# Optimization experiments

Measured on AMD Instinct MI355X. Metric: run time of the kernel, lower is better.

Reference implementation:

```python
import jax, jax.numpy as jnp
import numpy as np

N_HEADS = 8


def setup_inputs() -> dict:
    key = jax.random.key(0)
    k1, k2 = jax.random.split(key)
    image_qkv = jax.random.normal(k1, (2, 1536, 4096), dtype=jnp.float32)
    st_qkv = jax.random.normal(k2, (2, 1536, 1024), dtype=jnp.float32)
    return {"image_qkv": image_qkv, "st_qkv": st_qkv}


def reference(image_qkv, st_qkv):
    bs, width, img_len = image_qkv.shape
    st_len = st_qkv.shape[2]
    assert width % (3 * N_HEADS) == 0
    ch = width // (3 * N_HEADS)
    hc = N_HEADS * ch

    img_q, img_k, img_v = (image_qkv[:, i * hc:(i + 1) * hc] for i in range(3))
    st_q, st_k, st_v = (st_qkv[:, i * hc:(i + 1) * hc] for i in range(3))

    scale = 1.0 / jnp.sqrt(jnp.sqrt(jnp.float32(ch)))

    def split_heads(x, length):  # [bs, H*ch, L] -> [bs*H, ch, L]
        return x.reshape(bs * N_HEADS, ch, length)

    # image queries attend over st keys/values (softmax applied)
    w_i = jnp.einsum('bct,bcs->bts', split_heads(img_q, img_len) * scale,
                     split_heads(st_k, st_len) * scale)
    w_i = jax.nn.softmax(w_i.astype(jnp.float32), axis=-1).astype(w_i.dtype)
    attn_i = jnp.einsum('bts,bcs->bct', w_i, split_heads(st_v, st_len)).reshape(bs, -1, img_len)

    # st queries attend over image keys/values (NOTE: original code has NO softmax here)
    w_st = jnp.einsum('bct,bcs->bts', split_heads(st_q, st_len) * scale,
                      split_heads(img_k, img_len) * scale)
    attn_st = jnp.einsum('bts,bcs->bct', w_st, split_heads(img_v, img_len)).reshape(bs, -1, st_len)

    return attn_i, attn_st
```

## Files before the change

kernel.cpp:

```cpp
#include <hip/hip_runtime.h>
#include <hip/hip_bf16.h>
#include <stdint.h>

#define DEVI __device__ __forceinline__

typedef __attribute__((ext_vector_type(8))) short short8;
typedef __attribute__((ext_vector_type(16))) float f32x16;
typedef __attribute__((ext_vector_type(4))) float f32x4;
typedef __attribute__((ext_vector_type(2))) unsigned int uint2v;
typedef unsigned short ushortT;

union U8 { short8 s8; unsigned u[4]; };

DEVI unsigned short f2bf(float f) {
  unsigned u = __builtin_bit_cast(unsigned, f);
  u += 0x7fffu + ((u >> 16) & 1u);
  return (unsigned short)(u >> 16);
}
DEVI unsigned pk2(float lo, float hi) {
  return (unsigned)f2bf(lo) | ((unsigned)f2bf(hi) << 16);
}
DEVI unsigned cvtpk(float lo, float hi) {
  unsigned r;
  asm("v_cvt_pk_bf16_f32 %0, %1, %2" : "=v"(r) : "v"(lo), "v"(hi));
  return r;
}
DEVI float exp2a(float x) { return __builtin_amdgcn_exp2f(x); }

#define MFMA32 __builtin_amdgcn_mfma_f32_32x32x16_bf16
#define C_L2E 0.18033688011112042f

__global__ __launch_bounds__(256) void aux_kernel(
    const float* __restrict__ img, const float* __restrict__ st,
    ushortT* __restrict__ kfp, ushortT* __restrict__ vfp,
    float* __restrict__ Mws) {
  __shared__ __align__(16) char pool[32768];
  const int tid = threadIdx.x;
  const int bid = blockIdx.x;
  const int w = tid >> 6, lane = tid & 63, hi = lane >> 5, ln = lane & 31;

  if (bid < 256) {
    const int bh = bid >> 4, t = bid & 15;
    const int b = bh >> 3, h = bh & 7;
    const float* kbase = st + ((size_t)(b * 1536 + 512 + h * 64)) * 1024;
    const float* vbase = st + ((size_t)(b * 1536 + 1024 + h * 64)) * 1024;
    ushortT* ko = kfp + ((size_t)bh * 16 + t) * 4096;
    ushortT* vo = vfp + ((size_t)bh * 16 + t) * 4096;

    float (*kf)[65] = (float (*)[65])pool;
    {
      const int c = tid >> 2, s16 = (tid & 3) * 16;
      const float* kp = kbase + (size_t)c * 1024 + t * 64 + s16;
      f32x4 a = *(const f32x4*)kp, b4 = *(const f32x4*)(kp + 4),
            c4 = *(const f32x4*)(kp + 8), d4 = *(const f32x4*)(kp + 12);
#pragma unroll
      for (int j = 0; j < 4; ++j) {
        kf[c][s16 + j] = a[j];
        kf[c][s16 + 4 + j] = b4[j];
        kf[c][s16 + 8 + j] = c4[j];
        kf[c][s16 + 12 + j] = d4[j];
      }
    }
#pragma unroll
    for (int rep = 0; rep < 2; ++rep) {
      const int pair = tid + rep * 256;
      const int c = pair >> 3, oct = pair & 7;
      const float* vp = vbase + (size_t)c * 1024 + t * 64 + oct * 8;
      f32x4 lo = *(const f32x4*)vp, hp = *(const f32x4*)(vp + 4);
      uint2v la, ha;
      la[0] = pk2(lo[0], lo[1]); la[1] = pk2(lo[2], lo[3]);
      ha[0] = pk2(hp[0], hp[1]); ha[1] = pk2(hp[2], hp[3]);
      const int ci = c >> 5, lnn = c & 31;
      const int ss = oct >> 2, kk2 = (oct >> 1) & 1, o1 = oct & 1;
      const int f = ss * 4 + kk2 * 2 + ci;
      *(uint2v*)(vo + ((size_t)f * 64 + lnn) * 8 + o1 * 4) = la;
      *(uint2v*)(vo + ((size_t)f * 64 + 32 + lnn) * 8 + o1 * 4) = ha;
    }
    __syncthreads();
    {
      const int kk = w;
#pragma unroll
      for (int half = 0; half < 2; ++half) {
        float v8[8];
#pragma unroll
        for (int j = 0; j < 8; ++j) v8[j] = kf[kk * 16 + hi * 8 + j][half * 32 + ln];
        U8 u;
#pragma unroll
        for (int i = 0; i < 4; ++i) u.u[i] = pk2(v8[2 * i], v8[2 * i + 1]);
        *(short8*)(ko + ((size_t)(half * 4 + kk) * 64 + lane) * 8) = u.s8;
      }
    }
  } else {
    const int gb = bid - 256;
    const int bh = gb >> 3, chunk = gb & 7;
    const int b = bh >> 3, h = bh & 7;
    const float* kbase = img + ((size_t)(b * 1536 + 512 + h * 64)) * 4096;
    const float* vbase = img + ((size_t)(b * 1536 + 1024 + h * 64)) * 4096;

    f32x16 m00 = {}, m01 = {}, m10 = {}, m11 = {};
    const int sbeg = chunk * 512 + w * 128;
    for (int s0 = sbeg; s0 < sbeg + 128; s0 += 16) {
      const int sa = s0 + hi * 8;
      short8 av[2], bk[2];
#pragma unroll
      for (int ci = 0; ci < 2; ++ci) {
        const float* vp = vbase + (size_t)(ci * 32 + ln) * 4096 + sa;
        f32x4 lo = *(const f32x4*)vp, hp = *(const f32x4*)(vp + 4);
        U8 u;
        u.u[0] = pk2(lo[0], lo[1]); u.u[1] = pk2(lo[2], lo[3]);
        u.u[2] = pk2(hp[0], hp[1]); u.u[3] = pk2(hp[2], hp[3]);
        av[ci] = u.s8;
      }
#pragma unroll
      for (int cj = 0; cj < 2; ++cj) {
        const float* kp = kbase + (size_t)(cj * 32 + ln) * 4096 + sa;
        f32x4 lo = *(const f32x4*)kp, hp = *(const f32x4*)(kp + 4);
        U8 u;
        u.u[0] = pk2(lo[0], lo[1]); u.u[1] = pk2(lo[2], lo[3]);
        u.u[2] = pk2(hp[0], hp[1]); u.u[3] = pk2(hp[2], hp[3]);
        bk[cj] = u.s8;
      }
      m00 = MFMA32(av[0], bk[0], m00, 0, 0, 0);
      m01 = MFMA32(av[0], bk[1], m01, 0, 0, 0);
      m10 = MFMA32(av[1], bk[0], m10, 0, 0, 0);
      m11 = MFMA32(av[1], bk[1], m11, 0, 0, 0);
    }

    float (*part)[64][64] = (float (*)[64][64])pool;
    if (w < 2) {
#pragma unroll
      for (int q = 0; q < 16; ++q) {
        const int cr = (q & 3) + 8 * (q >> 2) + 4 * hi;
        part[w][cr][ln] = m00[q];
        part[w][cr][32 + ln] = m01[q];
        part[w][32 + cr][ln] = m10[q];
        part[w][32 + cr][32 + ln] = m11[q];
      }
    }
    __syncthreads();
    if (w >= 2) {
      const int pw = w - 2;
#pragma unroll
      for (int q = 0; q < 16; ++q) {
        const int cr = (q & 3) + 8 * (q >> 2) + 4 * hi;
        part[pw][cr][ln] += m00[q];
        part[pw][cr][32 + ln] += m01[q];
        part[pw][32 + cr][ln] += m10[q];
        part[pw][32 + cr][32 + ln] += m11[q];
      }
    }
    __syncthreads();
#pragma unroll
    for (int i = 0; i < 16; ++i) {
      const int e = tid + i * 256;
      const int c = e >> 6, cp = e & 63;
      Mws[(size_t)gb * 4096 + c * 64 + cp] =
          (part[0][c][cp] + part[1][c][cp]) * 0.125f;
    }
  }
}

DEVI void stage_tile(ushortT (*lds)[16][512], int buf, const ushortT* kf_all,
                     const ushortT* vf_all, int fpbase, int lane, int tile) {
#pragma unroll
  for (int j = 0; j < 4; ++j) {
    const int fp = fpbase + j;
    const ushortT* src =
        (fp < 8 ? kf_all + (size_t)tile * 4096 + (size_t)fp * 512
                : vf_all + (size_t)tile * 4096 + (size_t)(fp - 8) * 512) +
        lane * 8;
    __builtin_amdgcn_global_load_lds(
        (const __attribute__((address_space(1))) void*)src,
        (__attribute__((address_space(3))) void*)&lds[buf][fp][0], 16, 0, 0);
  }
}

DEVI void st2_body(const float* __restrict__ st, const float* __restrict__ Mws,
                   float* __restrict__ out1, int sb, int tid, char* pool) {
  const int bh = sb >> 2, tt = sb & 3;
  const int b = bh >> 3, h = bh & 7;
  const float* qbase = st + ((size_t)(b * 1536 + h * 64)) * 1024;
  float* o1 = out1 + ((size_t)(b * 512 + h * 64)) * 1024;
  char* msb = pool;

#pragma unroll
  for (int i = 0; i < 16; ++i) {
    const int e = tid + i * 256;
    const int c = e >> 6, cp = e & 63;
    const float* mp = Mws + (size_t)bh * 8 * 4096 + c * 64 + cp;
    float s = 0.f;
#pragma unroll
    for (int ch = 0; ch < 8; ++ch) s += mp[(size_t)ch * 4096];
    *(float*)(msb + c * 256 + ((cp * 4) ^ ((c & 7) << 5))) = s;
  }
  __syncthreads();

  const int w = tid >> 6, lane = tid & 63, hi = lane >> 5, ln = lane & 31;

  short8 aM0[4], aM1[4];
#pragma unroll
  for (int k = 0; k < 4; ++k) {
#pragma unroll
    for (int ci = 0; ci < 2; ++ci) {
      const int row = ci * 32 + ln;
      const int bo = k * 64 + hi * 32;
      const char* rp = msb + row * 256;
      const int swz = (row & 7) << 5;
      f32x4 lo = *(const f32x4*)(rp + (bo ^ swz));
      f32x4 hp = *(const f32x4*)(rp + ((bo + 16) ^ swz));
      U8 u;
      u.u[0] = pk2(lo[0], lo[1]); u.u[1] = pk2(lo[2], lo[3]);
      u.u[2] = pk2(hp[0], hp[1]); u.u[3] = pk2(hp[2], hp[3]);
      if (ci) aM1[k] = u.s8; else aM0[k] = u.s8;
    }
  }

#pragma unroll
  for (int nt = 0; nt < 2; ++nt) {
    const int t = tt * 256 + w * 64 + nt * 32 + ln;
    short8 bq[4];
#pragma unroll
    for (int k = 0; k < 4; ++k) {
      const float* qp = qbase + (size_t)(k * 16 + hi * 8) * 1024 + t;
      float q8[8];
#pragma unroll
      for (int j = 0; j < 8; ++j) q8[j] = qp[(size_t)j * 1024];
      U8 u;
#pragma unroll
      for (int i = 0; i < 4; ++i) u.u[i] = pk2(q8[2 * i], q8[2 * i + 1]);
      bq[k] = u.s8;
    }
    f32x16 a0 = {}, a1 = {};
#pragma unroll
    for (int k = 0; k < 4; ++k) {
      a0 = MFMA32(aM0[k], bq[k], a0, 0, 0, 0);
      a1 = MFMA32(aM1[k], bq[k], a1, 0, 0, 0);
    }
#pragma unroll
    for (int q = 0; q < 16; ++q) {
      const int cr = (q & 3) + 8 * (q >> 2) + 4 * hi;
      o1[(size_t)cr * 1024 + t] = a0[q];
      o1[(size_t)(cr + 32) * 1024 + t] = a1[q];
    }
  }
}

template <bool WITH_ST2>
__global__ __launch_bounds__(256, 2) void main_kernel(
    const float* __restrict__ img, const ushortT* __restrict__ kfp,
    const ushortT* __restrict__ vfp, const float* __restrict__ st,
    const float* __restrict__ Mws, float* __restrict__ out0,
    float* __restrict__ out1) {
  __shared__ __align__(16) char pool[65536];
  const int tid = threadIdx.x;
  const int bid = blockIdx.x;

  if (WITH_ST2 && bid >= 512) {
    st2_body(st, Mws, out1, bid - 512, tid, pool);
    return;
  }

  const int w = tid >> 6, lane = tid & 63, hi = lane >> 5, ln = lane & 31;
  const int bh = bid >> 5, tb = bid & 31;
  const int b = bh >> 3, h = bh & 7;
  const float* qbase = img + ((size_t)(b * 1536 + h * 64)) * 4096;
  float* obase = out0 + ((size_t)(b * 512 + h * 64)) * 4096;

  const int fpbase = w * 4;
  const int tcol = tb * 128 + w * 32 + ln;

  ushortT (*lds)[16][512] = (ushortT (*)[16][512])pool;
  const ushortT* kf_all = kfp + (size_t)bh * 16 * 4096;
  const ushortT* vf_all = vfp + (size_t)bh * 16 * 4096;

  stage_tile(lds, 0, kf_all, vf_all, fpbase, lane, 0);
  stage_tile(lds, 1, kf_all, vf_all, fpbase, lane, 1);
  stage_tile(lds, 2, kf_all, vf_all, fpbase, lane, 2);

  short8 qf[4];
#pragma unroll
  for (int k = 0; k < 4; ++k) {
    const float* qp = qbase + (size_t)(k * 16 + hi * 8) * 4096 + tcol;
    float q8[8];
#pragma unroll
    for (int j = 0; j < 8; ++j) q8[j] = qp[(size_t)j * 4096] * C_L2E;
    U8 u;
#pragma unroll
    for (int i = 0; i < 4; ++i) u.u[i] = pk2(q8[2 * i], q8[2 * i + 1]);
    qf[k] = u.s8;
  }

  f32x16 o0 = {}, o1 = {};
  float la0 = 0.f, la1 = 0.f, la2 = 0.f, la3 = 0.f;

  __syncthreads();

  for (int i = 0; i < 16; ++i) {
    if (i + 3 < 16)
      stage_tile(lds, (i + 3) & 3, kf_all, vf_all, fpbase, lane, i + 3);

    const ushortT(*L)[512] = lds[i & 3];

    f32x16 sc0 = {}, sc1 = {};
    {
      short8 kfr[8];
#pragma unroll
      for (int f = 0; f < 8; ++f) kfr[f] = *(const short8*)&L[f][lane * 8];
      __builtin_amdgcn_s_setprio(1);
      sc0 = MFMA32(kfr[0], qf[0], sc0, 0, 0, 0);
      sc1 = MFMA32(kfr[4], qf[0], sc1, 0, 0, 0);
      sc0 = MFMA32(kfr[1], qf[1], sc0, 0, 0, 0);
      sc1 = MFMA32(kfr[5], qf[1], sc1, 0, 0, 0);
      sc0 = MFMA32(kfr[2], qf[2], sc0, 0, 0, 0);
      sc1 = MFMA32(kfr[6], qf[2], sc1, 0, 0, 0);
      sc0 = MFMA32(kfr[3], qf[3], sc0, 0, 0, 0);
      sc1 = MFMA32(kfr[7], qf[3], sc1, 0, 0, 0);
      __builtin_amdgcn_s_setprio(0);
    }

#pragma unroll
    for (int q = 0; q < 16; q += 4) {
      float p0 = exp2a(sc0[q]);
      float p1 = exp2a(sc0[q + 1]);
      float p2 = exp2a(sc0[q + 2]);
      float p3 = exp2a(sc0[q + 3]);
      sc0[q] = p0; sc0[q + 1] = p1; sc0[q + 2] = p2; sc0[q + 3] = p3;
      la0 += p0; la1 += p1; la2 += p2; la3 += p3;
    }
#pragma unroll
    for (int q = 0; q < 16; q += 4) {
      float p0 = exp2a(sc1[q]);
      float p1 = exp2a(sc1[q + 1]);
      float p2 = exp2a(sc1[q + 2]);
      float p3 = exp2a(sc1[q + 3]);
      sc1[q] = p0; sc1[q + 1] = p1; sc1[q + 2] = p2; sc1[q + 3] = p3;
      la0 += p0; la1 += p1; la2 += p2; la3 += p3;
    }

#pragma unroll
    for (int ss = 0; ss < 2; ++ss) {
      const f32x16& sc = ss ? sc1 : sc0;
      U8 B0, B1;
      B0.u[0] = cvtpk(sc[0], sc[1]);   B0.u[1] = cvtpk(sc[2], sc[3]);
      B0.u[2] = cvtpk(sc[4], sc[5]);   B0.u[3] = cvtpk(sc[6], sc[7]);
      B1.u[0] = cvtpk(sc[8], sc[9]);   B1.u[1] = cvtpk(sc[10], sc[11]);
      B1.u[2] = cvtpk(sc[12], sc[13]); B1.u[3] = cvtpk(sc[14], sc[15]);
      short8 v00 = *(const short8*)&L[8 + ss * 4 + 0][lane * 8];
      short8 v01 = *(const short8*)&L[8 + ss * 4 + 1][lane * 8];
      short8 v10 = *(const short8*)&L[8 + ss * 4 + 2][lane * 8];
      short8 v11 = *(const short8*)&L[8 + ss * 4 + 3][lane * 8];
      __builtin_amdgcn_s_setprio(1);
      o0 = MFMA32(v00, B0.s8, o0, 0, 0, 0);
      o1 = MFMA32(v01, B0.s8, o1, 0, 0, 0);
      o0 = MFMA32(v10, B1.s8, o0, 0, 0, 0);
      o1 = MFMA32(v11, B1.s8, o1, 0, 0, 0);
      __builtin_amdgcn_s_setprio(0);
    }

    if (i + 1 < 16) {
      asm volatile("s_waitcnt vmcnt(8)" ::: "memory");
      __builtin_amdgcn_s_barrier();
      __builtin_amdgcn_sched_barrier(0);
    }
  }

  float l = (la0 + la1) + (la2 + la3);
  l += __shfl_xor(l, 32);
  const float linv = 1.0f / l;
#pragma unroll
  for (int q = 0; q < 16; ++q) {
    const int c = (q & 3) + 8 * (q >> 2) + 4 * hi;
    obase[(size_t)c * 4096 + tcol] = o0[q] * linv;
    obase[(size_t)(c + 32) * 4096 + tcol] = o1[q] * linv;
  }
}

__global__ __launch_bounds__(256) void st2_kernel(
    const float* __restrict__ st, const float* __restrict__ Mws,
    float* __restrict__ out1) {
  __shared__ __align__(16) char pool[16384];
  st2_body(st, Mws, out1, blockIdx.x, threadIdx.x, pool);
}

extern "C" void kernel_launch(void* const* d_in, const int* in_sizes, int n_in,
                              void* d_out, int out_size, void* d_ws, size_t ws_size,
                              hipStream_t stream) {
  const float* img = (const float*)d_in[0];
  const float* st = (const float*)d_in[1];
  float* out0 = (float*)d_out;
  float* out1 = out0 + (size_t)2 * 512 * 4096;
  char* ws = (char*)d_ws;
  const size_t MB = 1u << 20;

  ushortT* kfp;
  ushortT* vfp;
  float* Ms;
  bool fits = ws_size >= 6 * MB;
  if (fits) {
    kfp = (ushortT*)ws; vfp = (ushortT*)(ws + 2 * MB); Ms = (float*)(ws + 4 * MB);
  } else {
    kfp = (ushortT*)out1; vfp = (ushortT*)((char*)out1 + 2 * MB);
    Ms = (float*)ws;
  }

  hipLaunchKernelGGL(aux_kernel, dim3(384), dim3(256), 0, stream, img, st, kfp,
                     vfp, Ms);
  if (fits) {
    hipLaunchKernelGGL((main_kernel<true>), dim3(576), dim3(256), 0, stream, img,
                       kfp, vfp, st, Ms, out0, out1);
  } else {
    hipLaunchKernelGGL((main_kernel<false>), dim3(512), dim3(256), 0, stream, img,
                       kfp, vfp, st, Ms, out0, out1);
    hipLaunchKernelGGL(st2_kernel, dim3(64), dim3(256), 0, stream, st, Ms, out1);
  }
}
```

Measured before the change: 45.60 us.

## Software-pipeline QK^T of the next tile against softmax and PV of the current

Restructures the attention loop so each step issues the score MFMAs for tile i+1 while the exp and PV MFMAs for tile i run. Score accumulators ping-pong between two register sets, and the loop is unrolled by two. The goal is to overlap the exp2 VALU work with matrix-core work. Because the next tile's K is now read one step earlier, the global-load wait is tightened from vmcnt(8) to vmcnt(4). The change raises register pressure and adds one unused score computation on the final step.

```diff
diff --git a/kernel.cpp b/kernel.cpp
--- a/kernel.cpp
+++ b/kernel.cpp
@@ -245,6 +245,78 @@
   }
 }
 
+DEVI void step_pipe(ushortT (*lds)[16][512], const ushortT* kf_all,
+                    const ushortT* vf_all, int fpbase, int lane, int i,
+                    const short8 (&qf)[4], f32x16& cA0, f32x16& cA1,
+                    f32x16& cB0, f32x16& cB1, f32x16& o0, f32x16& o1,
+                    float& la0, float& la1, float& la2, float& la3) {
+  if (i + 3 < 16)
+    stage_tile(lds, (i + 3) & 3, kf_all, vf_all, fpbase, lane, i + 3);
+
+  const ushortT(*Lc)[512] = lds[i & 3];
+  const ushortT(*Ln)[512] = lds[(i + 1) & 3];
+
+  short8 vf[8], kn[8];
+#pragma unroll
+  for (int f = 0; f < 8; ++f) vf[f] = *(const short8*)&Lc[8 + f][lane * 8];
+#pragma unroll
+  for (int f = 0; f < 8; ++f) kn[f] = *(const short8*)&Ln[f][lane * 8];
+
+#pragma unroll
+  for (int q = 0; q < 16; q += 4) {
+    float p0 = exp2a(cA0[q]);
+    float p1 = exp2a(cA0[q + 1]);
+    float p2 = exp2a(cA0[q + 2]);
+    float p3 = exp2a(cA0[q + 3]);
+    cA0[q] = p0; cA0[q + 1] = p1; cA0[q + 2] = p2; cA0[q + 3] = p3;
+    la0 += p0; la1 += p1; la2 += p2; la3 += p3;
+  }
+#pragma unroll
+  for (int q = 0; q < 16; q += 4) {
+    float p0 = exp2a(cA1[q]);
+    float p1 = exp2a(cA1[q + 1]);
+    float p2 = exp2a(cA1[q + 2]);
+    float p3 = exp2a(cA1[q + 3]);
+    cA1[q] = p0; cA1[q + 1] = p1; cA1[q + 2] = p2; cA1[q + 3] = p3;
+    la0 += p0; la1 += p1; la2 += p2; la3 += p3;
+  }
+
+  cB0 = (f32x16){};
+  cB1 = (f32x16){};
+  __builtin_amdgcn_s_setprio(1);
+  cB0 = MFMA32(kn[0], qf[0], cB0, 0, 0, 0);
+  cB1 = MFMA32(kn[4], qf[0], cB1, 0, 0, 0);
+  cB0 = MFMA32(kn[1], qf[1], cB0, 0, 0, 0);
+  cB1 = MFMA32(kn[5], qf[1], cB1, 0, 0, 0);
+  cB0 = MFMA32(kn[2], qf[2], cB0, 0, 0, 0);
+  cB1 = MFMA32(kn[6], qf[2], cB1, 0, 0, 0);
+  cB0 = MFMA32(kn[3], qf[3], cB0, 0, 0, 0);
+  cB1 = MFMA32(kn[7], qf[3], cB1, 0, 0, 0);
+  __builtin_amdgcn_s_setprio(0);
+
+#pragma unroll
+  for (int ss = 0; ss < 2; ++ss) {
+    const f32x16& sc = ss ? cA1 : cA0;
+    U8 B0, B1;
+    B0.u[0] = cvtpk(sc[0], sc[1]);   B0.u[1] = cvtpk(sc[2], sc[3]);
+    B0.u[2] = cvtpk(sc[4], sc[5]);   B0.u[3] = cvtpk(sc[6], sc[7]);
+    B1.u[0] = cvtpk(sc[8], sc[9]);   B1.u[1] = cvtpk(sc[10], sc[11]);
+    B1.u[2] = cvtpk(sc[12], sc[13]); B1.u[3] = cvtpk(sc[14], sc[15]);
+    __builtin_amdgcn_s_setprio(1);
+    o0 = MFMA32(vf[ss * 4 + 0], B0.s8, o0, 0, 0, 0);
+    o1 = MFMA32(vf[ss * 4 + 1], B0.s8, o1, 0, 0, 0);
+    o0 = MFMA32(vf[ss * 4 + 2], B1.s8, o0, 0, 0, 0);
+    o1 = MFMA32(vf[ss * 4 + 3], B1.s8, o1, 0, 0, 0);
+    __builtin_amdgcn_s_setprio(0);
+  }
+
+  if (i + 1 < 16) {
+    asm volatile("s_waitcnt vmcnt(4)" ::: "memory");
+    __builtin_amdgcn_s_barrier();
+    __builtin_amdgcn_sched_barrier(0);
+  }
+}
+
 template <bool WITH_ST2>
 __global__ __launch_bounds__(256, 2) void main_kernel(
     const float* __restrict__ img, const ushortT* __restrict__ kfp,
@@ -295,73 +367,28 @@
 
   __syncthreads();
 
-  for (int i = 0; i < 16; ++i) {
-    if (i + 3 < 16)
-      stage_tile(lds, (i + 3) & 3, kf_all, vf_all, fpbase, lane, i + 3);
-
-    const ushortT(*L)[512] = lds[i & 3];
-
-    f32x16 sc0 = {}, sc1 = {};
-    {
-      short8 kfr[8];
-#pragma unroll
-      for (int f = 0; f < 8; ++f) kfr[f] = *(const short8*)&L[f][lane * 8];
-      __builtin_amdgcn_s_setprio(1);
-      sc0 = MFMA32(kfr[0], qf[0], sc0, 0, 0, 0);
-      sc1 = MFMA32(kfr[4], qf[0], sc1, 0, 0, 0);
-      sc0 = MFMA32(kfr[1], qf[1], sc0, 0, 0, 0);
-      sc1 = MFMA32(kfr[5], qf[1], sc1, 0, 0, 0);
-      sc0 = MFMA32(kfr[2], qf[2], sc0, 0, 0, 0);
-      sc1 = MFMA32(kfr[6], qf[2], sc1, 0, 0, 0);
-      sc0 = MFMA32(kfr[3], qf[3], sc0, 0, 0, 0);
-      sc1 = MFMA32(kfr[7], qf[3], sc1, 0, 0, 0);
-      __builtin_amdgcn_s_setprio(0);
-    }
-
-#pragma unroll
-    for (int q = 0; q < 16; q += 4) {
-      float p0 = exp2a(sc0[q]);
-      float p1 = exp2a(sc0[q + 1]);
-      float p2 = exp2a(sc0[q + 2]);
-      float p3 = exp2a(sc0[q + 3]);
-      sc0[q] = p0; sc0[q + 1] = p1; sc0[q + 2] = p2; sc0[q + 3] = p3;
-      la0 += p0; la1 += p1; la2 += p2; la3 += p3;
-    }
-#pragma unroll
-    for (int q = 0; q < 16; q += 4) {
-      float p0 = exp2a(sc1[q]);
-      float p1 = exp2a(sc1[q + 1]);
-      float p2 = exp2a(sc1[q + 2]);
-      float p3 = exp2a(sc1[q + 3]);
-      sc1[q] = p0; sc1[q + 1] = p1; sc1[q + 2] = p2; sc1[q + 3] = p3;
-      la0 += p0; la1 += p1; la2 += p2; la3 += p3;
-    }
-
-#pragma unroll
-    for (int ss = 0; ss < 2; ++ss) {
-      const f32x16& sc = ss ? sc1 : sc0;
-      U8 B0, B1;
-      B0.u[0] = cvtpk(sc[0], sc[1]);   B0.u[1] = cvtpk(sc[2], sc[3]);
-      B0.u[2] = cvtpk(sc[4], sc[5]);   B0.u[3] = cvtpk(sc[6], sc[7]);
-      B1.u[0] = cvtpk(sc[8], sc[9]);   B1.u[1] = cvtpk(sc[10], sc[11]);
-      B1.u[2] = cvtpk(sc[12], sc[13]); B1.u[3] = cvtpk(sc[14], sc[15]);
-      short8 v00 = *(const short8*)&L[8 + ss * 4 + 0][lane * 8];
-      short8 v01 = *(const short8*)&L[8 + ss * 4 + 1][lane * 8];
-      short8 v10 = *(const short8*)&L[8 + ss * 4 + 2][lane * 8];
-      short8 v11 = *(const short8*)&L[8 + ss * 4 + 3][lane * 8];
-      __builtin_amdgcn_s_setprio(1);
-      o0 = MFMA32(v00, B0.s8, o0, 0, 0, 0);
-      o1 = MFMA32(v01, B0.s8, o1, 0, 0, 0);
-      o0 = MFMA32(v10, B1.s8, o0, 0, 0, 0);
-      o1 = MFMA32(v11, B1.s8, o1, 0, 0, 0);
-      __builtin_amdgcn_s_setprio(0);
-    }
-
-    if (i + 1 < 16) {
-      asm volatile("s_waitcnt vmcnt(8)" ::: "memory");
-      __builtin_amdgcn_s_barrier();
-      __builtin_amdgcn_sched_barrier(0);
-    }
+  f32x16 sA0 = {}, sA1 = {}, sB0 = {}, sB1 = {};
+  {
+    short8 k0[8];
+#pragma unroll
+    for (int f = 0; f < 8; ++f) k0[f] = *(const short8*)&lds[0][f][lane * 8];
+    __builtin_amdgcn_s_setprio(1);
+    sA0 = MFMA32(k0[0], qf[0], sA0, 0, 0, 0);
+    sA1 = MFMA32(k0[4], qf[0], sA1, 0, 0, 0);
+    sA0 = MFMA32(k0[1], qf[1], sA0, 0, 0, 0);
+    sA1 = MFMA32(k0[5], qf[1], sA1, 0, 0, 0);
+    sA0 = MFMA32(k0[2], qf[2], sA0, 0, 0, 0);
+    sA1 = MFMA32(k0[6], qf[2], sA1, 0, 0, 0);
+    sA0 = MFMA32(k0[3], qf[3], sA0, 0, 0, 0);
+    sA1 = MFMA32(k0[7], qf[3], sA1, 0, 0, 0);
+    __builtin_amdgcn_s_setprio(0);
+  }
+
+  for (int ii = 0; ii < 16; ii += 2) {
+    step_pipe(lds, kf_all, vf_all, fpbase, lane, ii, qf, sA0, sA1, sB0, sB1,
+              o0, o1, la0, la1, la2, la3);
+    step_pipe(lds, kf_all, vf_all, fpbase, lane, ii + 1, qf, sB0, sB1, sA0, sA1,
+              o0, o1, la0, la1, la2, la3);
   }
 
   float l = (la0 + la1) + (la2 + la3);
```

Result: no change. 45.36 us (-0.5%).

## Split key sequence across warps with per-warp LDS buffers and merge partials

Applied to the files above, without the earlier changes.

Each block now covers 64 query columns instead of 128, and the grid doubles. Two warp pairs each handle half of the key/value sequence (split-K), and each warp stages its own double-buffered K/V sub-tiles into private LDS, so the per-iteration block barriers go away. The two halves' partial outputs and row sums are merged through LDS at the end. This is meant to raise parallelism and remove barrier stalls, at the cost of more redundant Q loads, a final merge step and more blocks.

```diff
diff --git a/kernel.cpp b/kernel.cpp
--- a/kernel.cpp
+++ b/kernel.cpp
@@ -160,18 +160,22 @@
   }
 }
 
-DEVI void stage_tile(ushortT (*lds)[16][512], int buf, const ushortT* kf_all,
-                     const ushortT* vf_all, int fpbase, int lane, int tile) {
+DEVI void stage_sub(ushortT* mybuf, int buf, const ushortT* kt, const ushortT* vt,
+                    int half, int lane) {
+  ushortT* dst = mybuf + buf * 4096;
 #pragma unroll
   for (int j = 0; j < 4; ++j) {
-    const int fp = fpbase + j;
-    const ushortT* src =
-        (fp < 8 ? kf_all + (size_t)tile * 4096 + (size_t)fp * 512
-                : vf_all + (size_t)tile * 4096 + (size_t)(fp - 8) * 512) +
-        lane * 8;
+    const ushortT* src = kt + (size_t)(half * 4 + j) * 512 + lane * 8;
     __builtin_amdgcn_global_load_lds(
         (const __attribute__((address_space(1))) void*)src,
-        (__attribute__((address_space(3))) void*)&lds[buf][fp][0], 16, 0, 0);
+        (__attribute__((address_space(3))) void*)(dst + j * 512), 16, 0, 0);
+  }
+#pragma unroll
+  for (int j = 0; j < 4; ++j) {
+    const ushortT* src = vt + (size_t)(half * 4 + j) * 512 + lane * 8;
+    __builtin_amdgcn_global_load_lds(
+        (const __attribute__((address_space(1))) void*)src,
+        (__attribute__((address_space(3))) void*)(dst + (4 + j) * 512), 16, 0, 0);
   }
 }
 
@@ -255,27 +259,22 @@
   const int tid = threadIdx.x;
   const int bid = blockIdx.x;
 
-  if (WITH_ST2 && bid >= 512) {
-    st2_body(st, Mws, out1, bid - 512, tid, pool);
+  if (WITH_ST2 && bid >= 1024) {
+    st2_body(st, Mws, out1, bid - 1024, tid, pool);
     return;
   }
 
   const int w = tid >> 6, lane = tid & 63, hi = lane >> 5, ln = lane & 31;
-  const int bh = bid >> 5, tb = bid & 31;
+  const int tg = w & 1, sch = w >> 1;
+  const int bh = bid >> 6, tb = bid & 63;
   const int b = bh >> 3, h = bh & 7;
   const float* qbase = img + ((size_t)(b * 1536 + h * 64)) * 4096;
   float* obase = out0 + ((size_t)(b * 512 + h * 64)) * 4096;
-
-  const int fpbase = w * 4;
-  const int tcol = tb * 128 + w * 32 + ln;
-
-  ushortT (*lds)[16][512] = (ushortT (*)[16][512])pool;
-  const ushortT* kf_all = kfp + (size_t)bh * 16 * 4096;
-  const ushortT* vf_all = vfp + (size_t)bh * 16 * 4096;
-
-  stage_tile(lds, 0, kf_all, vf_all, fpbase, lane, 0);
-  stage_tile(lds, 1, kf_all, vf_all, fpbase, lane, 1);
-  stage_tile(lds, 2, kf_all, vf_all, fpbase, lane, 2);
+  const int tcol = tb * 64 + tg * 32 + ln;
+
+  ushortT* mybuf = (ushortT*)(pool + w * 16384);
+  const ushortT* kbh = kfp + (size_t)bh * 16 * 4096;
+  const ushortT* vbh = vfp + (size_t)bh * 16 * 4096;
 
   short8 qf[4];
 #pragma unroll
@@ -290,88 +289,93 @@
     qf[k] = u.s8;
   }
 
+  {
+    const int g0 = sch * 16, g1 = g0 + 1;
+    stage_sub(mybuf, 0, kbh + (size_t)(g0 >> 1) * 4096, vbh + (size_t)(g0 >> 1) * 4096,
+              g0 & 1, lane);
+    stage_sub(mybuf, 1, kbh + (size_t)(g1 >> 1) * 4096, vbh + (size_t)(g1 >> 1) * 4096,
+              g1 & 1, lane);
+  }
+
   f32x16 o0 = {}, o1 = {};
   float la0 = 0.f, la1 = 0.f, la2 = 0.f, la3 = 0.f;
 
-  __syncthreads();
-
+#pragma unroll
   for (int i = 0; i < 16; ++i) {
-    if (i + 3 < 16)
-      stage_tile(lds, (i + 3) & 3, kf_all, vf_all, fpbase, lane, i + 3);
-
-    const ushortT(*L)[512] = lds[i & 3];
-
-    f32x16 sc0 = {}, sc1 = {};
+    if (i < 15)
+      asm volatile("s_waitcnt vmcnt(8)" ::: "memory");
+    else
+      asm volatile("s_waitcnt vmcnt(0)" ::: "memory");
+
+    const ushortT* B = mybuf + (i & 1) * 4096;
+
+    f32x16 sc = {};
     {
-      short8 kfr[8];
-#pragma unroll
-      for (int f = 0; f < 8; ++f) kfr[f] = *(const short8*)&L[f][lane * 8];
-      __builtin_amdgcn_s_setprio(1);
-      sc0 = MFMA32(kfr[0], qf[0], sc0, 0, 0, 0);
-      sc1 = MFMA32(kfr[4], qf[0], sc1, 0, 0, 0);
-      sc0 = MFMA32(kfr[1], qf[1], sc0, 0, 0, 0);
-      sc1 = MFMA32(kfr[5], qf[1], sc1, 0, 0, 0);
-      sc0 = MFMA32(kfr[2], qf[2], sc0, 0, 0, 0);
-      sc1 = MFMA32(kfr[6], qf[2], sc1, 0, 0, 0);
-      sc0 = MFMA32(kfr[3], qf[3], sc0, 0, 0, 0);
-      sc1 = MFMA32(kfr[7], qf[3], sc1, 0, 0, 0);
-      __builtin_amdgcn_s_setprio(0);
+      short8 k0 = *(const short8*)(B + 0 * 512 + lane * 8);
+      short8 k1 = *(const short8*)(B + 1 * 512 + lane * 8);
+      short8 k2 = *(const short8*)(B + 2 * 512 + lane * 8);
+      short8 k3 = *(const short8*)(B + 3 * 512 + lane * 8);
+      sc = MFMA32(k0, qf[0], sc, 0, 0, 0);
+      sc = MFMA32(k1, qf[1], sc, 0, 0, 0);
+      sc = MFMA32(k2, qf[2], sc, 0, 0, 0);
+      sc = MFMA32(k3, qf[3], sc, 0, 0, 0);
     }
 
 #pragma unroll
     for (int q = 0; q < 16; q += 4) {
-      float p0 = exp2a(sc0[q]);
-      float p1 = exp2a(sc0[q + 1]);
-      float p2 = exp2a(sc0[q + 2]);
-      float p3 = exp2a(sc0[q + 3]);
-      sc0[q] = p0; sc0[q + 1] = p1; sc0[q + 2] = p2; sc0[q + 3] = p3;
+      float p0 = exp2a(sc[q]);
+      float p1 = exp2a(sc[q + 1]);
+      float p2 = exp2a(sc[q + 2]);
+      float p3 = exp2a(sc[q + 3]);
+      sc[q] = p0; sc[q + 1] = p1; sc[q + 2] = p2; sc[q + 3] = p3;
       la0 += p0; la1 += p1; la2 += p2; la3 += p3;
     }
-#pragma unroll
-    for (int q = 0; q < 16; q += 4) {
-      float p0 = exp2a(sc1[q]);
-      float p1 = exp2a(sc1[q + 1]);
-      float p2 = exp2a(sc1[q + 2]);
-      float p3 = exp2a(sc1[q + 3]);
-      sc1[q] = p0; sc1[q + 1] = p1; sc1[q + 2] = p2; sc1[q + 3] = p3;
-      la0 += p0; la1 += p1; la2 += p2; la3 += p3;
-    }
-
-#pragma unroll
-    for (int ss = 0; ss < 2; ++ss) {
-      const f32x16& sc = ss ? sc1 : sc0;
+
+    {
       U8 B0, B1;
       B0.u[0] = cvtpk(sc[0], sc[1]);   B0.u[1] = cvtpk(sc[2], sc[3]);
       B0.u[2] = cvtpk(sc[4], sc[5]);   B0.u[3] = cvtpk(sc[6], sc[7]);
       B1.u[0] = cvtpk(sc[8], sc[9]);   B1.u[1] = cvtpk(sc[10], sc[11]);
       B1.u[2] = cvtpk(sc[12], sc[13]); B1.u[3] = cvtpk(sc[14], sc[15]);
-      short8 v00 = *(const short8*)&L[8 + ss * 4 + 0][lane * 8];
-      short8 v01 = *(const short8*)&L[8 + ss * 4 + 1][lane * 8];
-      short8 v10 = *(const short8*)&L[8 + ss * 4 + 2][lane * 8];
-      short8 v11 = *(const short8*)&L[8 + ss * 4 + 3][lane * 8];
-      __builtin_amdgcn_s_setprio(1);
-      o0 = MFMA32(v00, B0.s8, o0, 0, 0, 0);
-      o1 = MFMA32(v01, B0.s8, o1, 0, 0, 0);
-      o0 = MFMA32(v10, B1.s8, o0, 0, 0, 0);
-      o1 = MFMA32(v11, B1.s8, o1, 0, 0, 0);
-      __builtin_amdgcn_s_setprio(0);
-    }
-
-    if (i + 1 < 16) {
-      asm volatile("s_waitcnt vmcnt(8)" ::: "memory");
-      __builtin_amdgcn_s_barrier();
-      __builtin_amdgcn_sched_barrier(0);
+      short8 v0 = *(const short8*)(B + 4 * 512 + lane * 8);
+      short8 v1 = *(const short8*)(B + 5 * 512 + lane * 8);
+      short8 v2 = *(const short8*)(B + 6 * 512 + lane * 8);
+      short8 v3 = *(const short8*)(B + 7 * 512 + lane * 8);
+      o0 = MFMA32(v0, B0.s8, o0, 0, 0, 0);
+      o1 = MFMA32(v1, B0.s8, o1, 0, 0, 0);
+      o0 = MFMA32(v2, B1.s8, o0, 0, 0, 0);
+      o1 = MFMA32(v3, B1.s8, o1, 0, 0, 0);
+    }
+
+    if (i + 2 < 16) {
+      const int g = sch * 16 + i + 2;
+      stage_sub(mybuf, i & 1, kbh + (size_t)(g >> 1) * 4096,
+                vbh + (size_t)(g >> 1) * 4096, g & 1, lane);
     }
   }
 
   float l = (la0 + la1) + (la2 + la3);
   l += __shfl_xor(l, 32);
-  const float linv = 1.0f / l;
-#pragma unroll
-  for (int q = 0; q < 16; ++q) {
-    const int c = (q & 3) + 8 * (q >> 2) + 4 * hi;
-    obase[(size_t)c * 4096 + tcol] = o0[q] * linv;
-    obase[(size_t)(c + 32) * 4096 + tcol] = o1[q] * linv;
+
+  __syncthreads();
+  float (*mrg)[64][33] = (float (*)[64][33])pool;
+  if (sch == 1) {
+#pragma unroll
+    for (int q = 0; q < 16; ++q) {
+      mrg[tg][lane][q] = o0[q];
+      mrg[tg][lane][16 + q] = o1[q];
+    }
+    mrg[tg][lane][32] = l;
+  }
+  __syncthreads();
+  if (sch == 0) {
+    const float linv = 1.0f / (l + mrg[tg][lane][32]);
+#pragma unroll
+    for (int q = 0; q < 16; ++q) {
+      const int c = (q & 3) + 8 * (q >> 2) + 4 * hi;
+      obase[(size_t)c * 4096 + tcol] = (o0[q] + mrg[tg][lane][q]) * linv;
+      obase[(size_t)(c + 32) * 4096 + tcol] = (o1[q] + mrg[tg][lane][16 + q]) * linv;
+    }
   }
 }
 
@@ -406,10 +410,10 @@
   hipLaunchKernelGGL(aux_kernel, dim3(384), dim3(256), 0, stream, img, st, kfp,
                      vfp, Ms);
   if (fits) {
-    hipLaunchKernelGGL((main_kernel<true>), dim3(576), dim3(256), 0, stream, img,
+    hipLaunchKernelGGL((main_kernel<true>), dim3(1088), dim3(256), 0, stream, img,
                        kfp, vfp, st, Ms, out0, out1);
   } else {
-    hipLaunchKernelGGL((main_kernel<false>), dim3(512), dim3(256), 0, stream, img,
+    hipLaunchKernelGGL((main_kernel<false>), dim3(1024), dim3(256), 0, stream, img,
                        kfp, vfp, st, Ms, out0, out1);
     hipLaunchKernelGGL(st2_kernel, dim3(64), dim3(256), 0, stream, st, Ms, out1);
   }
```

Result: slower. 48.27 us (+5.9%).

## Split image attention warps over key halves with two query tiles each, merge partials

Applied to the files above, without the earlier changes.

The image-query attention loop is restructured. Each warp now handles two 32-column query tiles and half of the key sequence, so every K/V fragment loaded from LDS feeds twice as many MFMAs. The outputs and softmax denominators from the two key halves are merged through LDS at the end. Staging drops from a 4-deep to a double-buffered scheme with full __syncthreads, and the software bf16 rounding is replaced with the hardware v_cvt_pk_bf16_f32 instruction throughout. The cost is more accumulator registers, which may lower occupancy, plus an extra merge pass.

```diff
diff --git a/kernel.cpp b/kernel.cpp
--- a/kernel.cpp
+++ b/kernel.cpp
@@ -12,14 +12,6 @@
 
 union U8 { short8 s8; unsigned u[4]; };
 
-DEVI unsigned short f2bf(float f) {
-  unsigned u = __builtin_bit_cast(unsigned, f);
-  u += 0x7fffu + ((u >> 16) & 1u);
-  return (unsigned short)(u >> 16);
-}
-DEVI unsigned pk2(float lo, float hi) {
-  return (unsigned)f2bf(lo) | ((unsigned)f2bf(hi) << 16);
-}
 DEVI unsigned cvtpk(float lo, float hi) {
   unsigned r;
   asm("v_cvt_pk_bf16_f32 %0, %1, %2" : "=v"(r) : "v"(lo), "v"(hi));
@@ -68,8 +60,8 @@
       const float* vp = vbase + (size_t)c * 1024 + t * 64 + oct * 8;
       f32x4 lo = *(const f32x4*)vp, hp = *(const f32x4*)(vp + 4);
       uint2v la, ha;
-      la[0] = pk2(lo[0], lo[1]); la[1] = pk2(lo[2], lo[3]);
-      ha[0] = pk2(hp[0], hp[1]); ha[1] = pk2(hp[2], hp[3]);
+      la[0] = cvtpk(lo[0], lo[1]); la[1] = cvtpk(lo[2], lo[3]);
+      ha[0] = cvtpk(hp[0], hp[1]); ha[1] = cvtpk(hp[2], hp[3]);
       const int ci = c >> 5, lnn = c & 31;
       const int ss = oct >> 2, kk2 = (oct >> 1) & 1, o1 = oct & 1;
       const int f = ss * 4 + kk2 * 2 + ci;
@@ -86,7 +78,7 @@
         for (int j = 0; j < 8; ++j) v8[j] = kf[kk * 16 + hi * 8 + j][half * 32 + ln];
         U8 u;
 #pragma unroll
-        for (int i = 0; i < 4; ++i) u.u[i] = pk2(v8[2 * i], v8[2 * i + 1]);
+        for (int i = 0; i < 4; ++i) u.u[i] = cvtpk(v8[2 * i], v8[2 * i + 1]);
         *(short8*)(ko + ((size_t)(half * 4 + kk) * 64 + lane) * 8) = u.s8;
       }
     }
@@ -107,8 +99,8 @@
         const float* vp = vbase + (size_t)(ci * 32 + ln) * 4096 + sa;
         f32x4 lo = *(const f32x4*)vp, hp = *(const f32x4*)(vp + 4);
         U8 u;
-        u.u[0] = pk2(lo[0], lo[1]); u.u[1] = pk2(lo[2], lo[3]);
-        u.u[2] = pk2(hp[0], hp[1]); u.u[3] = pk2(hp[2], hp[3]);
+        u.u[0] = cvtpk(lo[0], lo[1]); u.u[1] = cvtpk(lo[2], lo[3]);
+        u.u[2] = cvtpk(hp[0], hp[1]); u.u[3] = cvtpk(hp[2], hp[3]);
         av[ci] = u.s8;
       }
 #pragma unroll
@@ -116,8 +108,8 @@
         const float* kp = kbase + (size_t)(cj * 32 + ln) * 4096 + sa;
         f32x4 lo = *(const f32x4*)kp, hp = *(const f32x4*)(kp + 4);
         U8 u;
-        u.u[0] = pk2(lo[0], lo[1]); u.u[1] = pk2(lo[2], lo[3]);
-        u.u[2] = pk2(hp[0], hp[1]); u.u[3] = pk2(hp[2], hp[3]);
+        u.u[0] = cvtpk(lo[0], lo[1]); u.u[1] = cvtpk(lo[2], lo[3]);
+        u.u[2] = cvtpk(hp[0], hp[1]); u.u[3] = cvtpk(hp[2], hp[3]);
         bk[cj] = u.s8;
       }
       m00 = MFMA32(av[0], bk[0], m00, 0, 0, 0);
@@ -160,18 +152,22 @@
   }
 }
 
-DEVI void stage_tile(ushortT (*lds)[16][512], int buf, const ushortT* kf_all,
-                     const ushortT* vf_all, int fpbase, int lane, int tile) {
-#pragma unroll
-  for (int j = 0; j < 4; ++j) {
-    const int fp = fpbase + j;
-    const ushortT* src =
-        (fp < 8 ? kf_all + (size_t)tile * 4096 + (size_t)fp * 512
-                : vf_all + (size_t)tile * 4096 + (size_t)(fp - 8) * 512) +
-        lane * 8;
-    __builtin_amdgcn_global_load_lds(
-        (const __attribute__((address_space(1))) void*)src,
-        (__attribute__((address_space(3))) void*)&lds[buf][fp][0], 16, 0, 0);
+DEVI void stage_pair(ushortT (*lds)[2][16][512], int buf, const ushortT* kbh,
+                     const ushortT* vbh, int step, int fpbase, int lane) {
+#pragma unroll
+  for (int c = 0; c < 2; ++c) {
+    const int g = c * 8 + step;
+#pragma unroll
+    for (int j = 0; j < 4; ++j) {
+      const int fp = fpbase + j;
+      const ushortT* src =
+          (fp < 8 ? kbh + (size_t)g * 4096 + (size_t)fp * 512
+                  : vbh + (size_t)g * 4096 + (size_t)(fp - 8) * 512) +
+          lane * 8;
+      __builtin_amdgcn_global_load_lds(
+          (const __attribute__((address_space(1))) void*)src,
+          (__attribute__((address_space(3))) void*)&lds[c][buf][fp][0], 16, 0, 0);
+    }
   }
 }
 
@@ -209,8 +205,8 @@
       f32x4 lo = *(const f32x4*)(rp + (bo ^ swz));
       f32x4 hp = *(const f32x4*)(rp + ((bo + 16) ^ swz));
       U8 u;
-      u.u[0] = pk2(lo[0], lo[1]); u.u[1] = pk2(lo[2], lo[3]);
-      u.u[2] = pk2(hp[0], hp[1]); u.u[3] = pk2(hp[2], hp[3]);
+      u.u[0] = cvtpk(lo[0], lo[1]); u.u[1] = cvtpk(lo[2], lo[3]);
+      u.u[2] = cvtpk(hp[0], hp[1]); u.u[3] = cvtpk(hp[2], hp[3]);
       if (ci) aM1[k] = u.s8; else aM0[k] = u.s8;
     }
   }
@@ -227,7 +223,7 @@
       for (int j = 0; j < 8; ++j) q8[j] = qp[(size_t)j * 1024];
       U8 u;
 #pragma unroll
-      for (int i = 0; i < 4; ++i) u.u[i] = pk2(q8[2 * i], q8[2 * i + 1]);
+      for (int i = 0; i < 4; ++i) u.u[i] = cvtpk(q8[2 * i], q8[2 * i + 1]);
       bq[k] = u.s8;
     }
     f32x16 a0 = {}, a1 = {};
@@ -261,117 +257,168 @@
   }
 
   const int w = tid >> 6, lane = tid & 63, hi = lane >> 5, ln = lane & 31;
+  const int tg = w & 1, sch = w >> 1;
   const int bh = bid >> 5, tb = bid & 31;
   const int b = bh >> 3, h = bh & 7;
   const float* qbase = img + ((size_t)(b * 1536 + h * 64)) * 4096;
   float* obase = out0 + ((size_t)(b * 512 + h * 64)) * 4096;
 
   const int fpbase = w * 4;
-  const int tcol = tb * 128 + w * 32 + ln;
-
-  ushortT (*lds)[16][512] = (ushortT (*)[16][512])pool;
-  const ushortT* kf_all = kfp + (size_t)bh * 16 * 4096;
-  const ushortT* vf_all = vfp + (size_t)bh * 16 * 4096;
-
-  stage_tile(lds, 0, kf_all, vf_all, fpbase, lane, 0);
-  stage_tile(lds, 1, kf_all, vf_all, fpbase, lane, 1);
-  stage_tile(lds, 2, kf_all, vf_all, fpbase, lane, 2);
-
-  short8 qf[4];
+  const int tcolA = tb * 128 + tg * 64 + ln;
+
+  ushortT (*lds)[2][16][512] = (ushortT (*)[2][16][512])pool;
+  const ushortT* kbh = kfp + (size_t)bh * 16 * 4096;
+  const ushortT* vbh = vfp + (size_t)bh * 16 * 4096;
+
+  stage_pair(lds, 0, kbh, vbh, 0, fpbase, lane);
+
+  short8 qfA[4], qfB[4];
 #pragma unroll
   for (int k = 0; k < 4; ++k) {
-    const float* qp = qbase + (size_t)(k * 16 + hi * 8) * 4096 + tcol;
-    float q8[8];
-#pragma unroll
-    for (int j = 0; j < 8; ++j) q8[j] = qp[(size_t)j * 4096] * C_L2E;
-    U8 u;
-#pragma unroll
-    for (int i = 0; i < 4; ++i) u.u[i] = pk2(q8[2 * i], q8[2 * i + 1]);
-    qf[k] = u.s8;
-  }
-
-  f32x16 o0 = {}, o1 = {};
-  float la0 = 0.f, la1 = 0.f, la2 = 0.f, la3 = 0.f;
+    const float* qp = qbase + (size_t)(k * 16 + hi * 8) * 4096 + tcolA;
+    float qa[8], qb[8];
+#pragma unroll
+    for (int j = 0; j < 8; ++j) {
+      qa[j] = qp[(size_t)j * 4096] * C_L2E;
+      qb[j] = qp[(size_t)j * 4096 + 32] * C_L2E;
+    }
+    U8 ua, ub;
+#pragma unroll
+    for (int i = 0; i < 4; ++i) {
+      ua.u[i] = cvtpk(qa[2 * i], qa[2 * i + 1]);
+      ub.u[i] = cvtpk(qb[2 * i], qb[2 * i + 1]);
+    }
+    qfA[k] = ua.s8;
+    qfB[k] = ub.s8;
+  }
+
+  f32x16 oA0 = {}, oA1 = {}, oB0 = {}, oB1 = {};
+  float laA0 = 0.f, laA1 = 0.f, laA2 = 0.f, laA3 = 0.f;
+  float laB0 = 0.f, laB1 = 0.f, laB2 = 0.f, laB3 = 0.f;
 
   __syncthreads();
 
-  for (int i = 0; i < 16; ++i) {
-    if (i + 3 < 16)
-      stage_tile(lds, (i + 3) & 3, kf_all, vf_all, fpbase, lane, i + 3);
-
-    const ushortT(*L)[512] = lds[i & 3];
-
-    f32x16 sc0 = {}, sc1 = {};
+  for (int i = 0; i < 8; ++i) {
+    const ushortT(*L)[512] = lds[sch][i & 1];
+
+    f32x16 sA0 = {}, sA1 = {}, sB0 = {}, sB1 = {};
     {
-      short8 kfr[8];
-#pragma unroll
-      for (int f = 0; f < 8; ++f) kfr[f] = *(const short8*)&L[f][lane * 8];
+      short8 kf[8];
+#pragma unroll
+      for (int f = 0; f < 8; ++f) kf[f] = *(const short8*)&L[f][lane * 8];
       __builtin_amdgcn_s_setprio(1);
-      sc0 = MFMA32(kfr[0], qf[0], sc0, 0, 0, 0);
-      sc1 = MFMA32(kfr[4], qf[0], sc1, 0, 0, 0);
-      sc0 = MFMA32(kfr[1], qf[1], sc0, 0, 0, 0);
-      sc1 = MFMA32(kfr[5], qf[1], sc1, 0, 0, 0);
-      sc0 = MFMA32(kfr[2], qf[2], sc0, 0, 0, 0);
-      sc1 = MFMA32(kfr[6], qf[2], sc1, 0, 0, 0);
-      sc0 = MFMA32(kfr[3], qf[3], sc0, 0, 0, 0);
-      sc1 = MFMA32(kfr[7], qf[3], sc1, 0, 0, 0);
+      sA0 = MFMA32(kf[0], qfA[0], sA0, 0, 0, 0);
+      sB0 = MFMA32(kf[0], qfB[0], sB0, 0, 0, 0);
+      sA1 = MFMA32(kf[4], qfA[0], sA1, 0, 0, 0);
+      sB1 = MFMA32(kf[4], qfB[0], sB1, 0, 0, 0);
+      sA0 = MFMA32(kf[1], qfA[1], sA0, 0, 0, 0);
+      sB0 = MFMA32(kf[1], qfB[1], sB0, 0, 0, 0);
+      sA1 = MFMA32(kf[5], qfA[1], sA1, 0, 0, 0);
+      sB1 = MFMA32(kf[5], qfB[1], sB1, 0, 0, 0);
+      sA0 = MFMA32(kf[2], qfA[2], sA0, 0, 0, 0);
+      sB0 = MFMA32(kf[2], qfB[2], sB0, 0, 0, 0);
+      sA1 = MFMA32(kf[6], qfA[2], sA1, 0, 0, 0);
+      sB1 = MFMA32(kf[6], qfB[2], sB1, 0, 0, 0);
+      sA0 = MFMA32(kf[3], qfA[3], sA0, 0, 0, 0);
+      sB0 = MFMA32(kf[3], qfB[3], sB0, 0, 0, 0);
+      sA1 = MFMA32(kf[7], qfA[3], sA1, 0, 0, 0);
+      sB1 = MFMA32(kf[7], qfB[3], sB1, 0, 0, 0);
       __builtin_amdgcn_s_setprio(0);
     }
 
+    if (i + 1 < 8) stage_pair(lds, (i + 1) & 1, kbh, vbh, i + 1, fpbase, lane);
+
 #pragma unroll
     for (int q = 0; q < 16; q += 4) {
-      float p0 = exp2a(sc0[q]);
-      float p1 = exp2a(sc0[q + 1]);
-      float p2 = exp2a(sc0[q + 2]);
-      float p3 = exp2a(sc0[q + 3]);
-      sc0[q] = p0; sc0[q + 1] = p1; sc0[q + 2] = p2; sc0[q + 3] = p3;
-      la0 += p0; la1 += p1; la2 += p2; la3 += p3;
+      float p0 = exp2a(sA0[q]), p1 = exp2a(sA0[q + 1]);
+      float p2 = exp2a(sA0[q + 2]), p3 = exp2a(sA0[q + 3]);
+      sA0[q] = p0; sA0[q + 1] = p1; sA0[q + 2] = p2; sA0[q + 3] = p3;
+      laA0 += p0; laA1 += p1; laA2 += p2; laA3 += p3;
     }
 #pragma unroll
     for (int q = 0; q < 16; q += 4) {
-      float p0 = exp2a(sc1[q]);
-      float p1 = exp2a(sc1[q + 1]);
-      float p2 = exp2a(sc1[q + 2]);
-      float p3 = exp2a(sc1[q + 3]);
-      sc1[q] = p0; sc1[q + 1] = p1; sc1[q + 2] = p2; sc1[q + 3] = p3;
-      la0 += p0; la1 += p1; la2 += p2; la3 += p3;
+      float p0 = exp2a(sA1[q]), p1 = exp2a(sA1[q + 1]);
+      float p2 = exp2a(sA1[q + 2]), p3 = exp2a(sA1[q + 3]);
+      sA1[q] = p0; sA1[q + 1] = p1; sA1[q + 2] = p2; sA1[q + 3] = p3;
+      laA0 += p0; laA1 += p1; laA2 += p2; laA3 += p3;
+    }
+#pragma unroll
+    for (int q = 0; q < 16; q += 4) {
+      float p0 = exp2a(sB0[q]), p1 = exp2a(sB0[q + 1]);
+      float p2 = exp2a(sB0[q + 2]), p3 = exp2a(sB0[q + 3]);
+      sB0[q] = p0; sB0[q + 1] = p1; sB0[q + 2] = p2; sB0[q + 3] = p3;
+      laB0 += p0; laB1 += p1; laB2 += p2; laB3 += p3;
+    }
+#pragma unroll
+    for (int q = 0; q < 16; q += 4) {
+      float p0 = exp2a(sB1[q]), p1 = exp2a(sB1[q + 1]);
+      float p2 = exp2a(sB1[q + 2]), p3 = exp2a(sB1[q + 3]);
+      sB1[q] = p0; sB1[q + 1] = p1; sB1[q + 2] = p2; sB1[q + 3] = p3;
+      laB0 += p0; laB1 += p1; laB2 += p2; laB3 += p3;
     }
 
 #pragma unroll
     for (int ss = 0; ss < 2; ++ss) {
-      const f32x16& sc = ss ? sc1 : sc0;
-      U8 B0, B1;
-      B0.u[0] = cvtpk(sc[0], sc[1]);   B0.u[1] = cvtpk(sc[2], sc[3]);
-      B0.u[2] = cvtpk(sc[4], sc[5]);   B0.u[3] = cvtpk(sc[6], sc[7]);
-      B1.u[0] = cvtpk(sc[8], sc[9]);   B1.u[1] = cvtpk(sc[10], sc[11]);
-      B1.u[2] = cvtpk(sc[12], sc[13]); B1.u[3] = cvtpk(sc[14], sc[15]);
-      short8 v00 = *(const short8*)&L[8 + ss * 4 + 0][lane * 8];
-      short8 v01 = *(const short8*)&L[8 + ss * 4 + 1][lane * 8];
-      short8 v10 = *(const short8*)&L[8 + ss * 4 + 2][lane * 8];
-      short8 v11 = *(const short8*)&L[8 + ss * 4 + 3][lane * 8];
+      const f32x16& a = ss ? sA1 : sA0;
+      const f32x16& bb = ss ? sB1 : sB0;
+      U8 A0, A1, B0, B1;
+      A0.u[0] = cvtpk(a[0], a[1]);    A0.u[1] = cvtpk(a[2], a[3]);
+      A0.u[2] = cvtpk(a[4], a[5]);    A0.u[3] = cvtpk(a[6], a[7]);
+      A1.u[0] = cvtpk(a[8], a[9]);    A1.u[1] = cvtpk(a[10], a[11]);
+      A1.u[2] = cvtpk(a[12], a[13]);  A1.u[3] = cvtpk(a[14], a[15]);
+      B0.u[0] = cvtpk(bb[0], bb[1]);   B0.u[1] = cvtpk(bb[2], bb[3]);
+      B0.u[2] = cvtpk(bb[4], bb[5]);   B0.u[3] = cvtpk(bb[6], bb[7]);
+      B1.u[0] = cvtpk(bb[8], bb[9]);   B1.u[1] = cvtpk(bb[10], bb[11]);
+      B1.u[2] = cvtpk(bb[12], bb[13]); B1.u[3] = cvtpk(bb[14], bb[15]);
+      short8 v0 = *(const short8*)&L[8 + ss * 4 + 0][lane * 8];
+      short8 v1 = *(const short8*)&L[8 + ss * 4 + 1][lane * 8];
+      short8 v2 = *(const short8*)&L[8 + ss * 4 + 2][lane * 8];
+      short8 v3 = *(const short8*)&L[8 + ss * 4 + 3][lane * 8];
       __builtin_amdgcn_s_setprio(1);
-      o0 = MFMA32(v00, B0.s8, o0, 0, 0, 0);
-      o1 = MFMA32(v01, B0.s8, o1, 0, 0, 0);
-      o0 = MFMA32(v10, B1.s8, o0, 0, 0, 0);
-      o1 = MFMA32(v11, B1.s8, o1, 0, 0, 0);
+      oA0 = MFMA32(v0, A0.s8, oA0, 0, 0, 0);
+      oA1 = MFMA32(v1, A0.s8, oA1, 0, 0, 0);
+      oB0 = MFMA32(v0, B0.s8, oB0, 0, 0, 0);
+      oB1 = MFMA32(v1, B0.s8, oB1, 0, 0, 0);
+      oA0 = MFMA32(v2, A1.s8, oA0, 0, 0, 0);
+      oA1 = MFMA32(v3, A1.s8, oA1, 0, 0, 0);
+      oB0 = MFMA32(v2, B1.s8, oB0, 0, 0, 0);
+      oB1 = MFMA32(v3, B1.s8, oB1, 0, 0, 0);
       __builtin_amdgcn_s_setprio(0);
     }
-
-    if (i + 1 < 16) {
-      asm volatile("s_waitcnt vmcnt(8)" ::: "memory");
-      __builtin_amdgcn_s_barrier();
-      __builtin_amdgcn_sched_barrier(0);
-    }
-  }
-
-  float l = (la0 + la1) + (la2 + la3);
-  l += __shfl_xor(l, 32);
-  const float linv = 1.0f / l;
-#pragma unroll
-  for (int q = 0; q < 16; ++q) {
-    const int c = (q & 3) + 8 * (q >> 2) + 4 * hi;
-    obase[(size_t)c * 4096 + tcol] = o0[q] * linv;
-    obase[(size_t)(c + 32) * 4096 + tcol] = o1[q] * linv;
+    if (i + 1 < 8) __syncthreads();
+  }
+
+  float lA = (laA0 + laA1) + (laA2 + laA3);
+  lA += __shfl_xor(lA, 32);
+  float lB = (laB0 + laB1) + (laB2 + laB3);
+  lB += __shfl_xor(lB, 32);
+
+  __syncthreads();
+  float (*mrg)[64][66] = (float (*)[64][66])pool;
+  if (sch == 1) {
+#pragma unroll
+    for (int q = 0; q < 16; ++q) {
+      mrg[tg][lane][q] = oA0[q];
+      mrg[tg][lane][16 + q] = oA1[q];
+      mrg[tg][lane][32 + q] = oB0[q];
+      mrg[tg][lane][48 + q] = oB1[q];
+    }
+    mrg[tg][lane][64] = lA;
+    mrg[tg][lane][65] = lB;
+  }
+  __syncthreads();
+  if (sch == 0) {
+    const float liA = 1.0f / (lA + mrg[tg][lane][64]);
+    const float liB = 1.0f / (lB + mrg[tg][lane][65]);
+#pragma unroll
+    for (int q = 0; q < 16; ++q) {
+      const int c = (q & 3) + 8 * (q >> 2) + 4 * hi;
+      obase[(size_t)c * 4096 + tcolA] = (oA0[q] + mrg[tg][lane][q]) * liA;
+      obase[(size_t)(c + 32) * 4096 + tcolA] = (oA1[q] + mrg[tg][lane][16 + q]) * liA;
+      obase[(size_t)c * 4096 + tcolA + 32] = (oB0[q] + mrg[tg][lane][32 + q]) * liB;
+      obase[(size_t)(c + 32) * 4096 + tcolA + 32] =
+          (oB1[q] + mrg[tg][lane][48 + q]) * liB;
+    }
   }
 }
 
```

Result: faster. 43.90 us, median of 3 (-3.7%).
